# Performance work log

Measured on AMD Instinct MI355X. Metric: run time of the kernel, lower is better.

Reference implementation:

```python
import jax, jax.numpy as jnp
import numpy as np

H_SP, W_SP = 8, 8
NUM_HEADS = 6
SHARED = 96
DIM_Q, DIM_KV = 96, 192
WIN = H_SP * W_SP  # 64 tokens per window


def _rel_index():
    # Swin-style relative position index, static numpy computation
    coords = np.stack(np.meshgrid(np.arange(H_SP), np.arange(W_SP), indexing='ij'))
    cf = coords.reshape(2, -1)                      # [2, 64]
    rel = cf[:, :, None] - cf[:, None, :]           # [2, 64, 64]
    rel = rel.transpose(1, 2, 0).astype(np.int64)   # [64, 64, 2]
    rel[..., 0] += H_SP - 1
    rel[..., 1] += W_SP - 1
    rel[..., 0] *= 2 * W_SP - 1
    return rel.sum(-1)                              # [64, 64], values in [0, 225)

REL_IDX = jnp.asarray(_rel_index())


def setup_inputs() -> dict:
    key = jax.random.key(0)
    ks = jax.random.split(key, 12)
    B, H, W = 4, 256, 256
    f32 = jnp.float32
    std = 0.02
    return {
        'x_q':  jax.random.normal(ks[0], (B, DIM_Q, H, W), f32),
        'x_kv': jax.random.normal(ks[1], (B, DIM_KV, H, W), f32),
        'Wq': jax.random.normal(ks[2], (DIM_Q, SHARED), f32) * std,
        'bq': jnp.zeros((SHARED,), f32),
        'Wk': jax.random.normal(ks[3], (DIM_KV, SHARED), f32) * std,
        'bk': jnp.zeros((SHARED,), f32),
        'Wv': jax.random.normal(ks[4], (DIM_KV, SHARED), f32) * std,
        'bv': jnp.zeros((SHARED,), f32),
        'bias_table': jax.random.normal(ks[5], ((2 * H_SP - 1) * (2 * W_SP - 1), NUM_HEADS), f32) * std,
        'Wo': jax.random.normal(ks[6], (SHARED, DIM_Q), f32) * std,
        'bo': jnp.zeros((DIM_Q,), f32),
    }


def reference(x_q, x_kv, Wq, bq, Wk, bk, Wv, bv, bias_table, Wo, bo):
    B, Cq, H, W = x_q.shape
    nH, nW = H // H_SP, W // W_SP  # H, W divisible by window -> pad is a no-op
    hd = SHARED // NUM_HEADS
    scale = hd ** -0.5

    def to_windows(img):
        C = img.shape[1]
        x = img.reshape(B, C, nH, H_SP, nW, W_SP)
        return x.transpose(0, 2, 4, 3, 5, 1).reshape(-1, WIN, C)

    qw = to_windows(x_q)    # [nWin, 64, Cq]
    kvw = to_windows(x_kv)  # [nWin, 64, Ckv]

    def heads(x):
        return x.reshape(-1, WIN, NUM_HEADS, hd).transpose(0, 2, 1, 3)  # [nWin, h, 64, hd]

    q = heads(qw @ Wq + bq)
    k = heads(kvw @ Wk + bk)
    v = heads(kvw @ Wv + bv)

    attn = jnp.einsum('whqd,whkd->whqk', q, k) * scale  # [nWin, h, 64, 64]
    rel_bias = bias_table[REL_IDX].transpose(2, 0, 1)   # [h, 64, 64]
    attn = jax.nn.softmax(attn + rel_bias[None], axis=-1)

    out = jnp.einsum('whqk,whkd->whqd', attn, v)        # [nWin, h, 64, hd]
    out = out.transpose(0, 2, 1, 3).reshape(-1, WIN, SHARED)
    out = out @ Wo + bo                                 # [nWin, 64, Cq]

    # windows2img
    out = out.reshape(B, nH, nW, H_SP, W_SP, Cq)
    out = out.transpose(0, 1, 3, 2, 4, 5).reshape(B, H, W, Cq)
    return out.transpose(0, 3, 1, 2)  # [B, Cq, H, W]
```

## Files before the change

kernel.cpp:

```cpp
#include <hip/hip_runtime.h>

typedef short short8 __attribute__((ext_vector_type(8)));
typedef float f32x4 __attribute__((ext_vector_type(4)));
typedef unsigned short ushort;

#define MFMA(a, b, c) __builtin_amdgcn_mfma_f32_16x16x32_bf16(a, b, c, 0, 0, 0)

#define WS_WQT 0
#define WS_WKT 9216
#define WS_WVT 27648
#define WS_WOT 46080
#define WS_BIAS 55296
#define WS_TOTAL 56646

#define STR_A 104
#define U_A    0
#define U_VT   6656
#define STR_VT 72
#define U_PS   13568
#define U_BIAS 18176
#define U_TOTAL 19526

#define DPP_F(v, ctrl) __int_as_float(__builtin_amdgcn_update_dpp(0, __float_as_int(v), ctrl, 0xF, 0xF, true))

__device__ __forceinline__ ushort f2bf(float x) {
    unsigned u = __float_as_uint(x);
    u = (u + 0x7FFFu + ((u >> 16) & 1u)) >> 16;
    return (ushort)u;
}
__device__ __forceinline__ float bf2f(ushort u) {
    return __uint_as_float(((unsigned)u) << 16);
}

__global__ void prep_weights(const float* __restrict__ Wq, const float* __restrict__ Wk,
                             const float* __restrict__ Wv, const float* __restrict__ Wo,
                             const float* __restrict__ btab, ushort* __restrict__ ws) {
    int idx = blockIdx.x * 256 + threadIdx.x;
    if (idx < WS_WKT) {
        int f = idx >> 9, w = idx & 511, lane = w >> 3, j = w & 7;
        int nt = f / 3, kt = f % 3;
        int n = nt * 16 + (lane & 15), k = kt * 32 + (lane >> 4) * 8 + j;
        ws[idx] = f2bf(Wq[k * 96 + n]);
    } else if (idx < WS_WVT) {
        int t = idx - WS_WKT;
        int f = t >> 9, w = t & 511, lane = w >> 3, j = w & 7;
        int kt6 = f / 6, nt = f % 6;
        int n = nt * 16 + (lane & 15), k = kt6 * 32 + (lane >> 4) * 8 + j;
        ws[idx] = f2bf(Wk[k * 96 + n]);
    } else if (idx < WS_WOT) {
        int t = idx - WS_WVT;
        int f = t >> 9, w = t & 511, lane = w >> 3, j = w & 7;
        int kt6 = f / 6, nt = f % 6;
        int n = nt * 16 + (lane & 15), k = kt6 * 32 + (lane >> 4) * 8 + j;
        ws[idx] = f2bf(Wv[k * 96 + n]);
    } else if (idx < WS_BIAS) {
        int t = idx - WS_WOT;
        int f = t >> 9, w = t & 511, lane = w >> 3, j = w & 7;
        int nt = f / 3, kt = f % 3;
        int n = nt * 16 + (lane & 15), k = kt * 32 + (lane >> 4) * 8 + j;
        ws[idx] = f2bf(Wo[k * 96 + n]);
    } else if (idx < WS_TOTAL) {
        ws[idx] = f2bf(btab[idx - WS_BIAS]);
    }
}

__global__ __launch_bounds__(256, 4) void swin_attn(
    const float* __restrict__ xq, const float* __restrict__ xkv,
    const float* __restrict__ bq, const float* __restrict__ bk,
    const float* __restrict__ bv, const float* __restrict__ bo,
    const ushort* __restrict__ ws, float* __restrict__ out)
{
    __shared__ __align__(16) ushort smem[U_TOTAL + 8];
    const int tid = threadIdx.x;
    const int wave = tid >> 6, lane = tid & 63;
    const int l15 = lane & 15, quad = lane >> 4;
    int wid = ((blockIdx.x & 7) << 9) | (blockIdx.x >> 3);
    const int b = wid >> 10;
    const int wh = (wid >> 5) & 31, ww = wid & 31;
    const int h0 = wh * 8, w0 = ww * 8;
    const int mt = wave;

    ushort* A     = smem + U_A;
    ushort* vt    = smem + U_VT;
    ushort* ps    = smem + U_PS + wave * 1152;
    ushort* qsc   = ps;
    ushort* biasl = smem + U_BIAS;

    float bqr[6], bkr[6], bvr[6];
    #pragma unroll
    for (int h = 0; h < 6; ++h) {
        bqr[h] = bq[h * 16 + l15]; bkr[h] = bk[h * 16 + l15]; bvr[h] = bv[h * 16 + l15];
    }

    int pc[3], pi[3];
    #pragma unroll
    for (int t = 0; t < 3; ++t) { int p = tid + t * 256; pc[t] = p % 96; pi[t] = p / 96; }

    const float* xqb = xq + (size_t)b * 96 * 65536;
    float4 pf[3][2];
    #pragma unroll
    for (int t = 0; t < 3; ++t) {
        const float* g = xqb + (size_t)pc[t] * 65536 + (h0 + pi[t]) * 256 + w0;
        pf[t][0] = *(const float4*)g; pf[t][1] = *(const float4*)(g + 4);
    }
    for (int i = tid; i < 1350; i += 256) biasl[i] = ws[WS_BIAS + i];

    #pragma unroll
    for (int t = 0; t < 3; ++t) {
        int base = (pi[t] * 8) * STR_A + pc[t];
        A[base]             = f2bf(pf[t][0].x); A[base + STR_A]     = f2bf(pf[t][0].y);
        A[base + 2 * STR_A] = f2bf(pf[t][0].z); A[base + 3 * STR_A] = f2bf(pf[t][0].w);
        A[base + 4 * STR_A] = f2bf(pf[t][1].x); A[base + 5 * STR_A] = f2bf(pf[t][1].y);
        A[base + 6 * STR_A] = f2bf(pf[t][1].z); A[base + 7 * STR_A] = f2bf(pf[t][1].w);
    }
    __syncthreads();

    const float* xkvb = xkv + (size_t)b * 192 * 65536;
    float4 pg[3][2];
    #pragma unroll
    for (int t = 0; t < 3; ++t) {
        const float* g = xkvb + (size_t)pc[t] * 65536 + (h0 + pi[t]) * 256 + w0;
        pg[t][0] = *(const float4*)g; pg[t][1] = *(const float4*)(g + 4);
    }

    const int arow = (mt * 16 + l15) * STR_A + quad * 8;
    short8 a0 = *(const short8*)(A + arow);
    short8 a1 = *(const short8*)(A + arow + 32);
    short8 a2 = *(const short8*)(A + arow + 64);
    unsigned qpk[12];
    #pragma unroll
    for (int h = 0; h < 6; ++h) {
        f32x4 qa = {bqr[h], bqr[h], bqr[h], bqr[h]};
        qa = MFMA(a0, *(const short8*)(ws + WS_WQT + ((h * 3 + 0) * 64 + lane) * 8), qa);
        qa = MFMA(a1, *(const short8*)(ws + WS_WQT + ((h * 3 + 1) * 64 + lane) * 8), qa);
        qa = MFMA(a2, *(const short8*)(ws + WS_WQT + ((h * 3 + 2) * 64 + lane) * 8), qa);
        qpk[h * 2]     = (unsigned)f2bf(qa[0] * 0.25f) | ((unsigned)f2bf(qa[1] * 0.25f) << 16);
        qpk[h * 2 + 1] = (unsigned)f2bf(qa[2] * 0.25f) | ((unsigned)f2bf(qa[3] * 0.25f) << 16);
    }
    __syncthreads();

    #pragma unroll
    for (int t = 0; t < 3; ++t) {
        int base = (pi[t] * 8) * STR_A + pc[t];
        A[base]             = f2bf(pg[t][0].x); A[base + STR_A]     = f2bf(pg[t][0].y);
        A[base + 2 * STR_A] = f2bf(pg[t][0].z); A[base + 3 * STR_A] = f2bf(pg[t][0].w);
        A[base + 4 * STR_A] = f2bf(pg[t][1].x); A[base + 5 * STR_A] = f2bf(pg[t][1].y);
        A[base + 6 * STR_A] = f2bf(pg[t][1].z); A[base + 7 * STR_A] = f2bf(pg[t][1].w);
    }
    __syncthreads();

    #pragma unroll
    for (int t = 0; t < 3; ++t) {
        const float* g = xkvb + (size_t)(96 + pc[t]) * 65536 + (h0 + pi[t]) * 256 + w0;
        pf[t][0] = *(const float4*)g; pf[t][1] = *(const float4*)(g + 4);
    }

    f32x4 accK[6], accV[6];
    #pragma unroll
    for (int n = 0; n < 6; ++n) {
        accK[n] = {bkr[n], bkr[n], bkr[n], bkr[n]};
        accV[n] = {bvr[n], bvr[n], bvr[n], bvr[n]};
    }
    #pragma unroll
    for (int kt = 0; kt < 3; ++kt) {
        short8 a = *(const short8*)(A + arow + kt * 32);
        #pragma unroll
        for (int nt = 0; nt < 6; ++nt) {
            short8 bk8 = *(const short8*)(ws + WS_WKT + (((kt * 6) + nt) * 64 + lane) * 8);
            accK[nt] = MFMA(a, bk8, accK[nt]);
            short8 bv8 = *(const short8*)(ws + WS_WVT + (((kt * 6) + nt) * 64 + lane) * 8);
            accV[nt] = MFMA(a, bv8, accV[nt]);
        }
    }
    __syncthreads();

    #pragma unroll
    for (int t = 0; t < 3; ++t) {
        int base = (pi[t] * 8) * STR_A + pc[t];
        A[base]             = f2bf(pf[t][0].x); A[base + STR_A]     = f2bf(pf[t][0].y);
        A[base + 2 * STR_A] = f2bf(pf[t][0].z); A[base + 3 * STR_A] = f2bf(pf[t][0].w);
        A[base + 4 * STR_A] = f2bf(pf[t][1].x); A[base + 5 * STR_A] = f2bf(pf[t][1].y);
        A[base + 6 * STR_A] = f2bf(pf[t][1].z); A[base + 7 * STR_A] = f2bf(pf[t][1].w);
    }
    __syncthreads();

    #pragma unroll
    for (int kt = 0; kt < 3; ++kt) {
        short8 a = *(const short8*)(A + arow + kt * 32);
        #pragma unroll
        for (int nt = 0; nt < 6; ++nt) {
            short8 bk8 = *(const short8*)(ws + WS_WKT + ((((3 + kt) * 6) + nt) * 64 + lane) * 8);
            accK[nt] = MFMA(a, bk8, accK[nt]);
            short8 bv8 = *(const short8*)(ws + WS_WVT + ((((3 + kt) * 6) + nt) * 64 + lane) * 8);
            accV[nt] = MFMA(a, bv8, accV[nt]);
        }
    }
    #pragma unroll
    for (int nt = 0; nt < 6; ++nt) {
        ushort* dk = A + (mt * 16 + quad * 4) * STR_A + nt * 16 + l15;
        ushort* dv = vt + nt * (16 * STR_VT) + l15 * STR_VT + (mt * 16 + quad * 4);
        #pragma unroll
        for (int r = 0; r < 4; ++r) {
            dk[r * STR_A] = f2bf(accK[nt][r]);
            dv[r]         = f2bf(accV[nt][r]);
        }
    }
    __syncthreads();

    const int qtok0 = mt * 16 + quad * 4;
    int bidx[4][4];
    #pragma unroll
    for (int nt = 0; nt < 4; ++nt) {
        int kt2 = nt * 16 + l15, i2 = kt2 >> 3, j2 = kt2 & 7;
        #pragma unroll
        for (int r = 0; r < 4; ++r) {
            int qt = qtok0 + r, i1 = qt >> 3, j1 = qt & 7;
            bidx[nt][r] = ((i1 - i2 + 7) * 15 + (j1 - j2 + 7)) * 6;
        }
    }

    f32x4 accO[6];
    short8 zero8 = {};
    #pragma unroll
    for (int h = 0; h < 6; ++h) {
        asm volatile("" ::: "memory");
        unsigned wlo = qpk[h * 2], whi = qpk[h * 2 + 1];
        qsc[(quad * 4 + 0) * 24 + l15] = (ushort)wlo;
        qsc[(quad * 4 + 1) * 24 + l15] = (ushort)(wlo >> 16);
        qsc[(quad * 4 + 2) * 24 + l15] = (ushort)whi;
        qsc[(quad * 4 + 3) * 24 + l15] = (ushort)(whi >> 16);
        short8 aq = zero8;
        if (quad < 2) aq = *(const short8*)(qsc + l15 * 24 + quad * 8);
        f32x4 s[4];
        #pragma unroll
        for (int nt = 0; nt < 4; ++nt) {
            short8 bk8 = zero8;
            if (quad < 2) bk8 = *(const short8*)(A + (nt * 16 + l15) * STR_A + h * 16 + quad * 8);
            f32x4 c;
            c[0] = bf2f(biasl[bidx[nt][0] + h]); c[1] = bf2f(biasl[bidx[nt][1] + h]);
            c[2] = bf2f(biasl[bidx[nt][2] + h]); c[3] = bf2f(biasl[bidx[nt][3] + h]);
            s[nt] = MFMA(aq, bk8, c);
        }
        float pr[4][4];
        #pragma unroll
        for (int r = 0; r < 4; ++r) {
            float m = fmaxf(fmaxf(s[0][r], s[1][r]), fmaxf(s[2][r], s[3][r]));
            m = fmaxf(m, DPP_F(m, 0xB1));
            m = fmaxf(m, DPP_F(m, 0x4E));
            m = fmaxf(m, DPP_F(m, 0x124));
            m = fmaxf(m, DPP_F(m, 0x128));
            float l = 0.f;
            #pragma unroll
            for (int nt = 0; nt < 4; ++nt) { pr[nt][r] = __expf(s[nt][r] - m); l += pr[nt][r]; }
            l += DPP_F(l, 0xB1); l += DPP_F(l, 0x4E);
            l += DPP_F(l, 0x124); l += DPP_F(l, 0x128);
            float inv = __builtin_amdgcn_rcpf(l);
            #pragma unroll
            for (int nt = 0; nt < 4; ++nt) pr[nt][r] *= inv;
        }
        #pragma unroll
        for (int nt = 0; nt < 4; ++nt)
            #pragma unroll
            for (int r = 0; r < 4; ++r)
                ps[(quad * 4 + r) * 72 + nt * 16 + l15] = f2bf(pr[nt][r]);
        f32x4 o = {};
        #pragma unroll
        for (int k2 = 0; k2 < 2; ++k2) {
            short8 ap  = *(const short8*)(ps + l15 * 72 + k2 * 32 + quad * 8);
            short8 bv8 = *(const short8*)(vt + h * (16 * STR_VT) + l15 * STR_VT + k2 * 32 + quad * 8);
            o = MFMA(ap, bv8, o);
        }
        accO[h] = o;
    }
    __syncthreads();

    float bor_[6];
    #pragma unroll
    for (int h = 0; h < 6; ++h) bor_[h] = bo[h * 16 + l15];
    ushort* obuf = A;
    #pragma unroll
    for (int h = 0; h < 6; ++h)
        #pragma unroll
        for (int r = 0; r < 4; ++r)
            obuf[(mt * 16 + quad * 4 + r) * STR_A + h * 16 + l15] = f2bf(accO[h][r]);

    {
        int t0 = mt * 16 + quad * 4;
        int i = t0 >> 3, j0 = t0 & 7;
        #pragma unroll
        for (int nt = 0; nt < 6; ++nt) {
            f32x4 acc = {bor_[nt], bor_[nt], bor_[nt], bor_[nt]};
            #pragma unroll
            for (int kt = 0; kt < 3; ++kt) {
                short8 a  = *(const short8*)(obuf + arow + kt * 32);
                short8 bb = *(const short8*)(ws + WS_WOT + ((nt * 3 + kt) * 64 + lane) * 8);
                acc = MFMA(a, bb, acc);
            }
            int cout = nt * 16 + l15;
            float4 v4 = make_float4(acc[0], acc[1], acc[2], acc[3]);
            float* dst = out + (size_t)(b * 96 + cout) * 65536 + (h0 + i) * 256 + w0 + j0;
            *(float4*)dst = v4;
        }
    }
}

extern "C" void kernel_launch(void* const* d_in, const int* in_sizes, int n_in,
                              void* d_out, int out_size, void* d_ws, size_t ws_size,
                              hipStream_t stream) {
    const float* xq   = (const float*)d_in[0];
    const float* xkv  = (const float*)d_in[1];
    const float* Wq   = (const float*)d_in[2];
    const float* bq   = (const float*)d_in[3];
    const float* Wk   = (const float*)d_in[4];
    const float* bk   = (const float*)d_in[5];
    const float* Wv   = (const float*)d_in[6];
    const float* bv   = (const float*)d_in[7];
    const float* btab = (const float*)d_in[8];
    const float* Wo   = (const float*)d_in[9];
    const float* bo   = (const float*)d_in[10];
    ushort* ws = (ushort*)d_ws;
    float* out = (float*)d_out;

    hipLaunchKernelGGL(prep_weights, dim3((WS_TOTAL + 255) / 256), dim3(256), 0, stream,
                       Wq, Wk, Wv, Wo, btab, ws);
    hipLaunchKernelGGL(swin_attn, dim3(4096), dim3(256), 0, stream,
                       xq, xkv, bq, bk, bv, bo, ws, out);
}
```

Before: 505.2 us.

## Software-pipeline weight loads, pair heads in attention loop, use exp2 softmax

Result: faster. 485.7 us (-3.9%).

```diff
diff --git a/kernel.cpp b/kernel.cpp
--- a/kernel.cpp
+++ b/kernel.cpp
@@ -20,6 +20,8 @@
 #define U_PS   13568
 #define U_BIAS 18176
 #define U_TOTAL 19526
+
+#define LOG2E 1.44269504f
 
 #define DPP_F(v, ctrl) __int_as_float(__builtin_amdgcn_update_dpp(0, __float_as_int(v), ctrl, 0xF, 0xF, true))
 
@@ -60,7 +62,26 @@
         int n = nt * 16 + (lane & 15), k = kt * 32 + (lane >> 4) * 8 + j;
         ws[idx] = f2bf(Wo[k * 96 + n]);
     } else if (idx < WS_TOTAL) {
-        ws[idx] = f2bf(btab[idx - WS_BIAS]);
+        ws[idx] = f2bf(btab[idx - WS_BIAS] * LOG2E);
+    }
+}
+
+__device__ __forceinline__ void softmax16(f32x4 (&s)[4], float (&pr)[4][4]) {
+    #pragma unroll
+    for (int r = 0; r < 4; ++r) {
+        float m = fmaxf(fmaxf(s[0][r], s[1][r]), fmaxf(s[2][r], s[3][r]));
+        m = fmaxf(m, DPP_F(m, 0xB1));
+        m = fmaxf(m, DPP_F(m, 0x4E));
+        m = fmaxf(m, DPP_F(m, 0x124));
+        m = fmaxf(m, DPP_F(m, 0x128));
+        float l = 0.f;
+        #pragma unroll
+        for (int nt = 0; nt < 4; ++nt) { pr[nt][r] = exp2f(s[nt][r] - m); l += pr[nt][r]; }
+        l += DPP_F(l, 0xB1); l += DPP_F(l, 0x4E);
+        l += DPP_F(l, 0x124); l += DPP_F(l, 0x128);
+        float inv = __builtin_amdgcn_rcpf(l);
+        #pragma unroll
+        for (int nt = 0; nt < 4; ++nt) pr[nt][r] *= inv;
     }
 }
 
@@ -83,7 +104,6 @@
     ushort* A     = smem + U_A;
     ushort* vt    = smem + U_VT;
     ushort* ps    = smem + U_PS + wave * 1152;
-    ushort* qsc   = ps;
     ushort* biasl = smem + U_BIAS;
 
     float bqr[6], bkr[6], bvr[6];
@@ -128,14 +148,26 @@
     short8 a1 = *(const short8*)(A + arow + 32);
     short8 a2 = *(const short8*)(A + arow + 64);
     unsigned qpk[12];
-    #pragma unroll
-    for (int h = 0; h < 6; ++h) {
-        f32x4 qa = {bqr[h], bqr[h], bqr[h], bqr[h]};
-        qa = MFMA(a0, *(const short8*)(ws + WS_WQT + ((h * 3 + 0) * 64 + lane) * 8), qa);
-        qa = MFMA(a1, *(const short8*)(ws + WS_WQT + ((h * 3 + 1) * 64 + lane) * 8), qa);
-        qa = MFMA(a2, *(const short8*)(ws + WS_WQT + ((h * 3 + 2) * 64 + lane) * 8), qa);
-        qpk[h * 2]     = (unsigned)f2bf(qa[0] * 0.25f) | ((unsigned)f2bf(qa[1] * 0.25f) << 16);
-        qpk[h * 2 + 1] = (unsigned)f2bf(qa[2] * 0.25f) | ((unsigned)f2bf(qa[3] * 0.25f) << 16);
+    {
+        short8 wq0 = *(const short8*)(ws + WS_WQT + ((0) * 64 + lane) * 8);
+        short8 wq1 = *(const short8*)(ws + WS_WQT + ((1) * 64 + lane) * 8);
+        short8 wq2 = *(const short8*)(ws + WS_WQT + ((2) * 64 + lane) * 8);
+        #pragma unroll
+        for (int h = 0; h < 6; ++h) {
+            short8 c0 = wq0, c1 = wq1, c2 = wq2;
+            if (h < 5) {
+                wq0 = *(const short8*)(ws + WS_WQT + (((h + 1) * 3 + 0) * 64 + lane) * 8);
+                wq1 = *(const short8*)(ws + WS_WQT + (((h + 1) * 3 + 1) * 64 + lane) * 8);
+                wq2 = *(const short8*)(ws + WS_WQT + (((h + 1) * 3 + 2) * 64 + lane) * 8);
+            }
+            f32x4 qa = {bqr[h], bqr[h], bqr[h], bqr[h]};
+            qa = MFMA(a0, c0, qa);
+            qa = MFMA(a1, c1, qa);
+            qa = MFMA(a2, c2, qa);
+            const float qs = 0.25f * LOG2E;
+            qpk[h * 2]     = (unsigned)f2bf(qa[0] * qs) | ((unsigned)f2bf(qa[1] * qs) << 16);
+            qpk[h * 2 + 1] = (unsigned)f2bf(qa[2] * qs) | ((unsigned)f2bf(qa[3] * qs) << 16);
+        }
     }
     __syncthreads();
 
@@ -149,12 +181,6 @@
     }
     __syncthreads();
 
-    #pragma unroll
-    for (int t = 0; t < 3; ++t) {
-        const float* g = xkvb + (size_t)(96 + pc[t]) * 65536 + (h0 + pi[t]) * 256 + w0;
-        pf[t][0] = *(const float4*)g; pf[t][1] = *(const float4*)(g + 4);
-    }
-
     f32x4 accK[6], accV[6];
     #pragma unroll
     for (int n = 0; n < 6; ++n) {
@@ -164,13 +190,22 @@
     #pragma unroll
     for (int kt = 0; kt < 3; ++kt) {
         short8 a = *(const short8*)(A + arow + kt * 32);
-        #pragma unroll
-        for (int nt = 0; nt < 6; ++nt) {
-            short8 bk8 = *(const short8*)(ws + WS_WKT + (((kt * 6) + nt) * 64 + lane) * 8);
-            accK[nt] = MFMA(a, bk8, accK[nt]);
-            short8 bv8 = *(const short8*)(ws + WS_WVT + (((kt * 6) + nt) * 64 + lane) * 8);
-            accV[nt] = MFMA(a, bv8, accV[nt]);
-        }
+        short8 wkf[6], wvf[6];
+        #pragma unroll
+        for (int nt = 0; nt < 6; ++nt)
+            wkf[nt] = *(const short8*)(ws + WS_WKT + (((kt * 6) + nt) * 64 + lane) * 8);
+        #pragma unroll
+        for (int nt = 0; nt < 6; ++nt)
+            wvf[nt] = *(const short8*)(ws + WS_WVT + (((kt * 6) + nt) * 64 + lane) * 8);
+        #pragma unroll
+        for (int nt = 0; nt < 6; ++nt) accK[nt] = MFMA(a, wkf[nt], accK[nt]);
+        #pragma unroll
+        for (int nt = 0; nt < 6; ++nt) accV[nt] = MFMA(a, wvf[nt], accV[nt]);
+    }
+    #pragma unroll
+    for (int t = 0; t < 3; ++t) {
+        const float* g = xkvb + (size_t)(96 + pc[t]) * 65536 + (h0 + pi[t]) * 256 + w0;
+        pf[t][0] = *(const float4*)g; pf[t][1] = *(const float4*)(g + 4);
     }
     __syncthreads();
 
@@ -187,13 +222,17 @@
     #pragma unroll
     for (int kt = 0; kt < 3; ++kt) {
         short8 a = *(const short8*)(A + arow + kt * 32);
-        #pragma unroll
-        for (int nt = 0; nt < 6; ++nt) {
-            short8 bk8 = *(const short8*)(ws + WS_WKT + ((((3 + kt) * 6) + nt) * 64 + lane) * 8);
-            accK[nt] = MFMA(a, bk8, accK[nt]);
-            short8 bv8 = *(const short8*)(ws + WS_WVT + ((((3 + kt) * 6) + nt) * 64 + lane) * 8);
-            accV[nt] = MFMA(a, bv8, accV[nt]);
-        }
+        short8 wkf[6], wvf[6];
+        #pragma unroll
+        for (int nt = 0; nt < 6; ++nt)
+            wkf[nt] = *(const short8*)(ws + WS_WKT + ((((3 + kt) * 6) + nt) * 64 + lane) * 8);
+        #pragma unroll
+        for (int nt = 0; nt < 6; ++nt)
+            wvf[nt] = *(const short8*)(ws + WS_WVT + ((((3 + kt) * 6) + nt) * 64 + lane) * 8);
+        #pragma unroll
+        for (int nt = 0; nt < 6; ++nt) accK[nt] = MFMA(a, wkf[nt], accK[nt]);
+        #pragma unroll
+        for (int nt = 0; nt < 6; ++nt) accV[nt] = MFMA(a, wvf[nt], accV[nt]);
     }
     #pragma unroll
     for (int nt = 0; nt < 6; ++nt) {
@@ -208,69 +247,95 @@
     __syncthreads();
 
     const int qtok0 = mt * 16 + quad * 4;
-    int bidx[4][4];
+    unsigned bidxp[4][2];
     #pragma unroll
     for (int nt = 0; nt < 4; ++nt) {
         int kt2 = nt * 16 + l15, i2 = kt2 >> 3, j2 = kt2 & 7;
+        unsigned v[4];
         #pragma unroll
         for (int r = 0; r < 4; ++r) {
             int qt = qtok0 + r, i1 = qt >> 3, j1 = qt & 7;
-            bidx[nt][r] = ((i1 - i2 + 7) * 15 + (j1 - j2 + 7)) * 6;
-        }
+            v[r] = (unsigned)(((i1 - i2 + 7) * 15 + (j1 - j2 + 7)) * 6);
+        }
+        bidxp[nt][0] = v[0] | (v[1] << 16);
+        bidxp[nt][1] = v[2] | (v[3] << 16);
     }
 
     f32x4 accO[6];
     short8 zero8 = {};
     #pragma unroll
-    for (int h = 0; h < 6; ++h) {
+    for (int hp = 0; hp < 3; ++hp) {
+        const int hA = hp * 2, hB = hA + 1;
         asm volatile("" ::: "memory");
-        unsigned wlo = qpk[h * 2], whi = qpk[h * 2 + 1];
-        qsc[(quad * 4 + 0) * 24 + l15] = (ushort)wlo;
-        qsc[(quad * 4 + 1) * 24 + l15] = (ushort)(wlo >> 16);
-        qsc[(quad * 4 + 2) * 24 + l15] = (ushort)whi;
-        qsc[(quad * 4 + 3) * 24 + l15] = (ushort)(whi >> 16);
-        short8 aq = zero8;
-        if (quad < 2) aq = *(const short8*)(qsc + l15 * 24 + quad * 8);
-        f32x4 s[4];
+        unsigned wloA = qpk[hA * 2], whiA = qpk[hA * 2 + 1];
+        unsigned wloB = qpk[hB * 2], whiB = qpk[hB * 2 + 1];
+        ps[(quad * 4 + 0) * 24 + l15] = (ushort)wloA;
+        ps[(quad * 4 + 1) * 24 + l15] = (ushort)(wloA >> 16);
+        ps[(quad * 4 + 2) * 24 + l15] = (ushort)whiA;
+        ps[(quad * 4 + 3) * 24 + l15] = (ushort)(whiA >> 16);
+        ps[384 + (quad * 4 + 0) * 24 + l15] = (ushort)wloB;
+        ps[384 + (quad * 4 + 1) * 24 + l15] = (ushort)(wloB >> 16);
+        ps[384 + (quad * 4 + 2) * 24 + l15] = (ushort)whiB;
+        ps[384 + (quad * 4 + 3) * 24 + l15] = (ushort)(whiB >> 16);
+        short8 aqA = zero8, aqB = zero8;
+        short8 kfA[4] = {zero8, zero8, zero8, zero8};
+        short8 kfB[4] = {zero8, zero8, zero8, zero8};
+        if (quad < 2) {
+            aqA = *(const short8*)(ps + l15 * 24 + quad * 8);
+            aqB = *(const short8*)(ps + 384 + l15 * 24 + quad * 8);
+            #pragma unroll
+            for (int nt = 0; nt < 4; ++nt) {
+                kfA[nt] = *(const short8*)(A + (nt * 16 + l15) * STR_A + hA * 16 + quad * 8);
+                kfB[nt] = *(const short8*)(A + (nt * 16 + l15) * STR_A + hB * 16 + quad * 8);
+            }
+        }
+        f32x4 sA[4], sB[4];
         #pragma unroll
         for (int nt = 0; nt < 4; ++nt) {
-            short8 bk8 = zero8;
-            if (quad < 2) bk8 = *(const short8*)(A + (nt * 16 + l15) * STR_A + h * 16 + quad * 8);
+            unsigned i01 = bidxp[nt][0], i23 = bidxp[nt][1];
             f32x4 c;
-            c[0] = bf2f(biasl[bidx[nt][0] + h]); c[1] = bf2f(biasl[bidx[nt][1] + h]);
-            c[2] = bf2f(biasl[bidx[nt][2] + h]); c[3] = bf2f(biasl[bidx[nt][3] + h]);
-            s[nt] = MFMA(aq, bk8, c);
-        }
-        float pr[4][4];
-        #pragma unroll
-        for (int r = 0; r < 4; ++r) {
-            float m = fmaxf(fmaxf(s[0][r], s[1][r]), fmaxf(s[2][r], s[3][r]));
-            m = fmaxf(m, DPP_F(m, 0xB1));
-            m = fmaxf(m, DPP_F(m, 0x4E));
-            m = fmaxf(m, DPP_F(m, 0x124));
-            m = fmaxf(m, DPP_F(m, 0x128));
-            float l = 0.f;
-            #pragma unroll
-            for (int nt = 0; nt < 4; ++nt) { pr[nt][r] = __expf(s[nt][r] - m); l += pr[nt][r]; }
-            l += DPP_F(l, 0xB1); l += DPP_F(l, 0x4E);
-            l += DPP_F(l, 0x124); l += DPP_F(l, 0x128);
-            float inv = __builtin_amdgcn_rcpf(l);
-            #pragma unroll
-            for (int nt = 0; nt < 4; ++nt) pr[nt][r] *= inv;
-        }
+            c[0] = bf2f(biasl[(i01 & 0xFFFFu) + hA]); c[1] = bf2f(biasl[(i01 >> 16) + hA]);
+            c[2] = bf2f(biasl[(i23 & 0xFFFFu) + hA]); c[3] = bf2f(biasl[(i23 >> 16) + hA]);
+            sA[nt] = MFMA(aqA, kfA[nt], c);
+        }
+        #pragma unroll
+        for (int nt = 0; nt < 4; ++nt) {
+            unsigned i01 = bidxp[nt][0], i23 = bidxp[nt][1];
+            f32x4 c;
+            c[0] = bf2f(biasl[(i01 & 0xFFFFu) + hB]); c[1] = bf2f(biasl[(i01 >> 16) + hB]);
+            c[2] = bf2f(biasl[(i23 & 0xFFFFu) + hB]); c[3] = bf2f(biasl[(i23 >> 16) + hB]);
+            sB[nt] = MFMA(aqB, kfB[nt], c);
+        }
+        float prA[4][4], prB[4][4];
+        softmax16(sA, prA);
+        softmax16(sB, prB);
+        asm volatile("" ::: "memory");
         #pragma unroll
         for (int nt = 0; nt < 4; ++nt)
             #pragma unroll
             for (int r = 0; r < 4; ++r)
-                ps[(quad * 4 + r) * 72 + nt * 16 + l15] = f2bf(pr[nt][r]);
-        f32x4 o = {};
+                ps[(quad * 4 + r) * 72 + nt * 16 + l15] = f2bf(prA[nt][r]);
+        f32x4 oA = {};
         #pragma unroll
         for (int k2 = 0; k2 < 2; ++k2) {
             short8 ap  = *(const short8*)(ps + l15 * 72 + k2 * 32 + quad * 8);
-            short8 bv8 = *(const short8*)(vt + h * (16 * STR_VT) + l15 * STR_VT + k2 * 32 + quad * 8);
-            o = MFMA(ap, bv8, o);
-        }
-        accO[h] = o;
+            short8 bv8 = *(const short8*)(vt + hA * (16 * STR_VT) + l15 * STR_VT + k2 * 32 + quad * 8);
+            oA = MFMA(ap, bv8, oA);
+        }
+        asm volatile("" ::: "memory");
+        #pragma unroll
+        for (int nt = 0; nt < 4; ++nt)
+            #pragma unroll
+            for (int r = 0; r < 4; ++r)
+                ps[(quad * 4 + r) * 72 + nt * 16 + l15] = f2bf(prB[nt][r]);
+        f32x4 oB = {};
+        #pragma unroll
+        for (int k2 = 0; k2 < 2; ++k2) {
+            short8 ap  = *(const short8*)(ps + l15 * 72 + k2 * 32 + quad * 8);
+            short8 bv8 = *(const short8*)(vt + hB * (16 * STR_VT) + l15 * STR_VT + k2 * 32 + quad * 8);
+            oB = MFMA(ap, bv8, oB);
+        }
+        accO[hA] = oA; accO[hB] = oB;
     }
     __syncthreads();
 
@@ -287,15 +352,24 @@
     {
         int t0 = mt * 16 + quad * 4;
         int i = t0 >> 3, j0 = t0 & 7;
+        short8 oa0 = *(const short8*)(obuf + arow);
+        short8 oa1 = *(const short8*)(obuf + arow + 32);
+        short8 oa2 = *(const short8*)(obuf + arow + 64);
+        short8 wo0 = *(const short8*)(ws + WS_WOT + ((0) * 64 + lane) * 8);
+        short8 wo1 = *(const short8*)(ws + WS_WOT + ((1) * 64 + lane) * 8);
+        short8 wo2 = *(const short8*)(ws + WS_WOT + ((2) * 64 + lane) * 8);
         #pragma unroll
         for (int nt = 0; nt < 6; ++nt) {
+            short8 c0 = wo0, c1 = wo1, c2 = wo2;
+            if (nt < 5) {
+                wo0 = *(const short8*)(ws + WS_WOT + (((nt + 1) * 3 + 0) * 64 + lane) * 8);
+                wo1 = *(const short8*)(ws + WS_WOT + (((nt + 1) * 3 + 1) * 64 + lane) * 8);
+                wo2 = *(const short8*)(ws + WS_WOT + (((nt + 1) * 3 + 2) * 64 + lane) * 8);
+            }
             f32x4 acc = {bor_[nt], bor_[nt], bor_[nt], bor_[nt]};
-            #pragma unroll
-            for (int kt = 0; kt < 3; ++kt) {
-                short8 a  = *(const short8*)(obuf + arow + kt * 32);
-                short8 bb = *(const short8*)(ws + WS_WOT + ((nt * 3 + kt) * 64 + lane) * 8);
-                acc = MFMA(a, bb, acc);
-            }
+            acc = MFMA(oa0, c0, acc);
+            acc = MFMA(oa1, c1, acc);
+            acc = MFMA(oa2, c2, acc);
             int cout = nt * 16 + l15;
             float4 v4 = make_float4(acc[0], acc[1], acc[2], acc[3]);
             float* dst = out + (size_t)(b * 96 + cout) * 65536 + (h0 + i) * 256 + w0 + j0;
```
